# Performance work log

Measured on AMD Instinct MI355X. Metric: run time of the kernel, lower is better.

Reference implementation:

```python
import jax, jax.numpy as jnp
import numpy as np

WS = 8          # window size
DIM = 512       # midplanes
HEADS = 16      # 512 // 32
HD = DIM // HEADS
SCALE = HD ** -0.5
EPS = 1e-5      # BatchNorm eps


def _rel_index():
    # Swin-style relative position index, (WS*WS, WS*WS) int32, static.
    coords = np.stack(np.meshgrid(np.arange(WS), np.arange(WS), indexing='ij')).reshape(2, -1)
    rel = (coords[:, :, None] - coords[:, None, :]).transpose(1, 2, 0)
    rel[..., 0] += WS - 1
    rel[..., 1] += WS - 1
    rel[..., 0] *= 2 * WS - 1
    return jnp.asarray(rel.sum(-1), dtype=jnp.int32)

REL_IDX = _rel_index()


def _bn(x, gamma, beta, mean, var):
    # eval-mode BatchNorm2d on (B, C, H, W)
    inv = jax.lax.rsqrt(var + EPS)
    return (x - mean[None, :, None, None]) * (inv * gamma)[None, :, None, None] + beta[None, :, None, None]


def _forward(x, qkv_w, qkv_b, proj_w, proj_b, rel_bias_table,
             bn1_gamma, bn1_beta, bn1_mean, bn1_var,
             mlp_w1, mlp_b1, mlp_w2, mlp_b2,
             bn2_gamma, bn2_beta, bn2_mean, bn2_var):
    B, C, H, W = x.shape
    Hb, Wb = H // WS, W // WS
    shortcut = x

    xn = _bn(x, bn1_gamma, bn1_beta, bn1_mean, bn1_var)

    # window_partition (islocal=True): (B,C,H,W) -> (B*nW, WS*WS, C)
    xw = xn.reshape(B, C, Hb, WS, Wb, WS).transpose(0, 2, 4, 3, 5, 1).reshape(-1, WS * WS, C)

    # WindowAttention
    B_, N, _ = xw.shape
    qkv = xw @ qkv_w + qkv_b                       # (B_, N, 3*C)
    qkv = qkv.reshape(B_, N, 3, HEADS, HD).transpose(2, 0, 3, 1, 4)
    q, k, v = qkv[0], qkv[1], qkv[2]               # (B_, H, N, HD)
    attn = jnp.einsum('bhnd,bhmd->bhnm', q * SCALE, k)
    bias = rel_bias_table[REL_IDX]                 # (N, N, HEADS)
    attn = attn + bias.transpose(2, 0, 1)[None]
    attn = jax.nn.softmax(attn, axis=-1)
    out = jnp.einsum('bhnm,bhmd->bhnd', attn, v).transpose(0, 2, 1, 3).reshape(B_, N, C)
    out = out @ proj_w + proj_b                    # (B_, N, C)

    # window_reverse (islocal=True) — replicate torch's .view reinterpretation exactly
    aw = out.reshape(-1, WS, WS, DIM)              # (B*nW, WS, WS, C) contiguous
    xr = aw.reshape(B, DIM, Hb, Wb, WS, WS)        # row-major reinterpret (as in torch .view)
    xr = xr.transpose(0, 1, 2, 4, 3, 5).reshape(B, DIM, H, W)

    x1 = shortcut + xr                             # drop_path is identity at eval

    # MLP of 1x1 convs
    xn2 = _bn(x1, bn2_gamma, bn2_beta, bn2_mean, bn2_var)
    h = jnp.einsum('oc,bchw->bohw', mlp_w1, xn2) + mlp_b1[None, :, None, None]
    h = jax.nn.gelu(h, approximate=False)
    h = jnp.einsum('oc,bchw->bohw', mlp_w2, h) + mlp_b2[None, :, None, None]
    return x1 + h


def setup_inputs() -> dict:
    key = jax.random.key(0)
    ks = jax.random.split(key, 12)
    B, H, W = 8, 128, 128
    s = 0.02
    return {
        'x': jax.random.normal(ks[0], (B, DIM, H, W), dtype=jnp.float32),
        'qkv_w': jax.random.normal(ks[1], (DIM, 3 * DIM), dtype=jnp.float32) * s,
        'qkv_b': jnp.zeros((3 * DIM,), jnp.float32),
        'proj_w': jax.random.normal(ks[2], (DIM, DIM), dtype=jnp.float32) * s,
        'proj_b': jnp.zeros((DIM,), jnp.float32),
        'rel_bias_table': jax.random.normal(ks[3], ((2 * WS - 1) ** 2, HEADS), dtype=jnp.float32) * s,
        'bn1_gamma': jnp.ones((DIM,), jnp.float32),
        'bn1_beta': jnp.zeros((DIM,), jnp.float32),
        'bn1_mean': jax.random.normal(ks[4], (DIM,), dtype=jnp.float32) * 0.1,
        'bn1_var': jax.random.uniform(ks[5], (DIM,), jnp.float32, 0.5, 1.5),
        'mlp_w1': jax.random.normal(ks[6], (DIM, DIM), dtype=jnp.float32) * s,
        'mlp_b1': jnp.zeros((DIM,), jnp.float32),
        'mlp_w2': jax.random.normal(ks[7], (DIM, DIM), dtype=jnp.float32) * s,
        'mlp_b2': jnp.zeros((DIM,), jnp.float32),
        'bn2_gamma': jnp.ones((DIM,), jnp.float32),
        'bn2_beta': jnp.zeros((DIM,), jnp.float32),
        'bn2_mean': jax.random.normal(ks[8], (DIM,), dtype=jnp.float32) * 0.1,
        'bn2_var': jax.random.uniform(ks[9], (DIM,), jnp.float32, 0.5, 1.5),
    }


def reference(x, qkv_w, qkv_b, proj_w, proj_b, rel_bias_table,
              bn1_gamma, bn1_beta, bn1_mean, bn1_var,
              mlp_w1, mlp_b1, mlp_w2, mlp_b2,
              bn2_gamma, bn2_beta, bn2_mean, bn2_var):
    return _forward(x, qkv_w, qkv_b, proj_w, proj_b, rel_bias_table,
                    bn1_gamma, bn1_beta, bn1_mean, bn1_var,
                    mlp_w1, mlp_b1, mlp_w2, mlp_b2,
                    bn2_gamma, bn2_beta, bn2_mean, bn2_var)
```

## Files before the change

kernel.cpp:

```cpp
#include <hip/hip_runtime.h>
#include <cstddef>


typedef unsigned short ushort_t;
typedef __attribute__((ext_vector_type(8))) short short8;
typedef __attribute__((ext_vector_type(4))) float float4v;

__device__ __forceinline__ float bf2f(unsigned short h) {
  union { unsigned int u; float f; } c; c.u = ((unsigned int)h) << 16; return c.f;
}
__device__ __forceinline__ unsigned short f2bf(float f) {
  union { float f; unsigned int u; } c; c.f = f;
  unsigned int u = c.u;
  unsigned int r = u + 0x7fffu + ((u >> 16) & 1u);
  return (unsigned short)(r >> 16);
}
__device__ __forceinline__ void async16(const void* g, void* l) {
  __builtin_amdgcn_global_load_lds(
      (const __attribute__((address_space(1))) unsigned int*)g,
      (__attribute__((address_space(3))) unsigned int*)l, 16, 0, 0);
}

__global__ void transpose_cast(const float* __restrict__ W, ushort_t* __restrict__ Wt,
                               int K, int N) {
  int idx = blockIdx.x * 256 + threadIdx.x;
  if (idx >= K * N) return;
  int nn = idx / K, kk = idx - nn * K;
  Wt[idx] = f2bf(W[(size_t)kk * N + nn]);
}
__global__ void cast_bf(const float* __restrict__ W, ushort_t* __restrict__ Wt, int total) {
  int idx = blockIdx.x * 256 + threadIdx.x;
  if (idx < total) Wt[idx] = f2bf(W[idx]);
}

__global__ __launch_bounds__(256) void prep_qkv(
    const float* __restrict__ x, const float* __restrict__ gamma,
    const float* __restrict__ beta, const float* __restrict__ mean,
    const float* __restrict__ var, ushort_t* __restrict__ A0) {
  const int w = blockIdx.x;
  const int cc0 = blockIdx.y << 5;
  const int b = w >> 8, hb = (w >> 4) & 15, wb = w & 15;
  __shared__ __align__(16) ushort_t tile[64][32];
  const int tid = threadIdx.x;
  const int ci = tid >> 3, row = tid & 7;
  const int c = cc0 + ci;
  const float a = gamma[c] * rsqrtf(var[c] + 1e-5f);
  const float sh = beta[c] - mean[c] * a;
  const float* xp = x + (((size_t)b * 512 + c) * 128 + (hb << 3) + row) * 128 + (wb << 3);
#pragma unroll
  for (int j = 0; j < 8; ++j) tile[(row << 3) + j][ci] = f2bf(xp[j] * a + sh);
  __syncthreads();
  const int n = tid >> 2, d0 = (tid & 3) << 3;
  *(uint4*)(A0 + (size_t)((w << 6) + n) * 512 + cc0 + d0) = *(const uint4*)&tile[n][d0];
}

template <int EPI>
__global__ __launch_bounds__(256) void gemm_bt(
    const ushort_t* __restrict__ A, const ushort_t* __restrict__ Bt,
    const float* __restrict__ bias, ushort_t* __restrict__ C,
    int M, int N, int K) {
  __shared__ __align__(16) ushort_t lA[128 * 32];
  __shared__ __align__(16) ushort_t lB[128 * 32];
  const int tid = threadIdx.x;
  const int wave = tid >> 6, lane = tid & 63;
  const int m0 = blockIdx.y << 7, n0 = blockIdx.x << 7;
  const int wm = (wave & 1) << 6, wn = (wave >> 1) << 6;

  float4v acc[4][4];
#pragma unroll
  for (int i = 0; i < 4; ++i)
#pragma unroll
    for (int j = 0; j < 4; ++j)
#pragma unroll
      for (int r = 0; r < 4; ++r) acc[i][j][r] = 0.0f;

  const int srow = (wave << 5) + (lane >> 2);
  const int skb = (lane & 3) << 3;
  const ushort_t* Ag = A + (size_t)(m0 + srow) * K + skb;
  const ushort_t* Bg = Bt + (size_t)(n0 + srow) * K + skb;
  ushort_t* lA0 = &lA[(wave << 5) * 32];
  ushort_t* lA1 = &lA[((wave << 5) + 16) * 32];
  ushort_t* lB0 = &lB[(wave << 5) * 32];
  ushort_t* lB1 = &lB[((wave << 5) + 16) * 32];
  const int fr = lane & 15;
  const int fk = (lane >> 4) << 3;

  for (int kt = 0; kt < K; kt += 32) {
    async16(Ag + kt, lA0);
    async16(Ag + kt + (size_t)16 * K, lA1);
    async16(Bg + kt, lB0);
    async16(Bg + kt + (size_t)16 * K, lB1);
    __syncthreads();
    short8 af[4], bfr[4];
#pragma unroll
    for (int i = 0; i < 4; ++i) {
      af[i] = *(const short8*)&lA[(wm + (i << 4) + fr) * 32 + fk];
      bfr[i] = *(const short8*)&lB[(wn + (i << 4) + fr) * 32 + fk];
    }
#pragma unroll
    for (int i = 0; i < 4; ++i)
#pragma unroll
      for (int j = 0; j < 4; ++j)
        acc[i][j] = __builtin_amdgcn_mfma_f32_16x16x32_bf16(af[i], bfr[j], acc[i][j], 0, 0, 0);
    __syncthreads();
  }

  const int cr = (lane >> 4) << 2;
  const int cc = lane & 15;
#pragma unroll
  for (int j = 0; j < 4; ++j) {
    const int col = n0 + wn + (j << 4) + cc;
    const float bv = bias[col];
#pragma unroll
    for (int i = 0; i < 4; ++i) {
      size_t base = (size_t)(m0 + wm + (i << 4) + cr) * N + col;
#pragma unroll
      for (int r = 0; r < 4; ++r) {
        float v = acc[i][j][r] + bv;
        if (EPI == 1) v = 0.5f * v * (1.0f + erff(v * 0.70710678118654752f));
        C[base + (size_t)r * N] = f2bf(v);
      }
    }
  }
}

__global__ __launch_bounds__(256) void attn_kernel(
    const ushort_t* __restrict__ QKV, const float* __restrict__ table,
    ushort_t* __restrict__ OUT) {
  const int w = blockIdx.x;
  const int h = blockIdx.y;
  __shared__ __align__(16) ushort_t Vt[32][72];
  __shared__ __align__(16) ushort_t Pw[4][16][72];
  __shared__ float bias_s[225];
  const int tid = threadIdx.x;
  const int wave = tid >> 6, lane = tid & 63;
  const int g = lane >> 4, c = lane & 15;

  if (tid < 225) bias_s[tid] = table[tid * 16 + h];

  const ushort_t* base = QKV + (size_t)(w << 6) * 1536 + h * 32;

  {
    uint4 vv = *(const uint4*)(base + (size_t)lane * 1536 + 1024 + (wave << 3));
    const ushort_t* vp = (const ushort_t*)&vv;
#pragma unroll
    for (int e = 0; e < 8; ++e) Vt[(wave << 3) + e][lane] = vp[e];
  }

  short8 qf = *(const short8*)(base + (size_t)((wave << 4) + c) * 1536 + (g << 3));
  short8 kf[4];
#pragma unroll
  for (int j = 0; j < 4; ++j)
    kf[j] = *(const short8*)(base + (size_t)((j << 4) + c) * 1536 + 512 + (g << 3));

  float4v acc[4];
#pragma unroll
  for (int j = 0; j < 4; ++j) {
#pragma unroll
    for (int r = 0; r < 4; ++r) acc[j][r] = 0.0f;
    acc[j] = __builtin_amdgcn_mfma_f32_16x16x32_bf16(qf, kf[j], acc[j], 0, 0, 0);
  }

  __syncthreads();

  const int q0 = (wave << 4) + (g << 2);
#pragma unroll
  for (int j = 0; j < 4; ++j) {
    const int k = (j << 4) + c;
    const int r2 = k >> 3, c2 = k & 7;
#pragma unroll
    for (int r = 0; r < 4; ++r) {
      const int q = q0 + r;
      const int idx = ((q >> 3) - r2 + 7) * 15 + ((q & 7) - c2 + 7);
      acc[j][r] = acc[j][r] * 0.17677669529663689f + bias_s[idx];
    }
  }

#pragma unroll
  for (int r = 0; r < 4; ++r) {
    float m = fmaxf(fmaxf(acc[0][r], acc[1][r]), fmaxf(acc[2][r], acc[3][r]));
    m = fmaxf(m, __shfl_xor(m, 1));
    m = fmaxf(m, __shfl_xor(m, 2));
    m = fmaxf(m, __shfl_xor(m, 4));
    m = fmaxf(m, __shfl_xor(m, 8));
    float s = 0.0f;
#pragma unroll
    for (int j = 0; j < 4; ++j) { acc[j][r] = __expf(acc[j][r] - m); s += acc[j][r]; }
    s += __shfl_xor(s, 1);
    s += __shfl_xor(s, 2);
    s += __shfl_xor(s, 4);
    s += __shfl_xor(s, 8);
    const float inv = 1.0f / s;
#pragma unroll
    for (int j = 0; j < 4; ++j)
      Pw[wave][(g << 2) + r][(j << 4) + c] = f2bf(acc[j][r] * inv);
  }

  __syncthreads();

  float4v oacc[2];
#pragma unroll
  for (int j2 = 0; j2 < 2; ++j2)
#pragma unroll
    for (int r = 0; r < 4; ++r) oacc[j2][r] = 0.0f;
#pragma unroll
  for (int ks = 0; ks < 2; ++ks) {
    short8 pa = *(const short8*)&Pw[wave][c][(ks << 5) + (g << 3)];
#pragma unroll
    for (int j2 = 0; j2 < 2; ++j2) {
      short8 vb = *(const short8*)&Vt[(j2 << 4) + c][(ks << 5) + (g << 3)];
      oacc[j2] = __builtin_amdgcn_mfma_f32_16x16x32_bf16(pa, vb, oacc[j2], 0, 0, 0);
    }
  }

  ushort_t* op = OUT + (size_t)((w << 6) + (wave << 4)) * 512 + h * 32;
#pragma unroll
  for (int j2 = 0; j2 < 2; ++j2)
#pragma unroll
    for (int r = 0; r < 4; ++r)
      op[(size_t)((g << 2) + r) * 512 + (j2 << 4) + c] = f2bf(oacc[j2][r]);
}

__device__ __forceinline__ size_t scramble_idx(int b, int F) {
  const int hb0 = F >> 19, wb0 = (F >> 15) & 15;
  const int rr = (F >> 12) & 7, ccol = (F >> 9) & 7, ch = F & 511;
  return ((size_t)(b * 256 + hb0 * 16 + wb0) * 64 + rr * 8 + ccol) * 512 + ch;
}

__global__ __launch_bounds__(256) void prep_mlp(
    const float* __restrict__ x, const ushort_t* __restrict__ PROJ,
    const float* __restrict__ gamma, const float* __restrict__ beta,
    const float* __restrict__ mean, const float* __restrict__ var,
    ushort_t* __restrict__ XN2) {
  const int pc = blockIdx.x;
  const int cc0 = blockIdx.y << 5;
  const int p0 = pc << 6;
  const int b = p0 >> 14, hh = (p0 >> 7) & 127;
  __shared__ __align__(16) ushort_t tile[64][32];
  const int tid = threadIdx.x;
  const int ci = tid >> 3, wg = (tid & 7) << 3;
  const int c = cc0 + ci;
  const float a = gamma[c] * rsqrtf(var[c] + 1e-5f);
  const float sh = beta[c] - mean[c] * a;
  const int w0 = (p0 & 127) + wg;
  const float* xp = x + (((size_t)b * 512 + c) * 128 + hh) * 128 + w0;
  const int hb = hh >> 3, r2 = hh & 7;
#pragma unroll
  for (int j = 0; j < 8; ++j) {
    const int ww = w0 + j;
    const int F = (c << 14) + (hb << 10) + ((ww >> 3) << 6) + (r2 << 3) + (ww & 7);
    const float x1 = xp[j] + bf2f(PROJ[scramble_idx(b, F)]);
    tile[wg + j][ci] = f2bf(x1 * a + sh);
  }
  __syncthreads();
  const int i2 = tid >> 2, d0 = (tid & 3) << 3;
  *(uint4*)(XN2 + (size_t)(p0 + i2) * 512 + cc0 + d0) = *(const uint4*)&tile[i2][d0];
}

__global__ __launch_bounds__(256) void final_add(
    const float* __restrict__ x, const ushort_t* __restrict__ PROJ,
    const ushort_t* __restrict__ H2, float* __restrict__ out) {
  const int pc = blockIdx.x, cc0 = blockIdx.y << 5;
  const int p0 = pc << 6;
  const int b = p0 >> 14, hh = (p0 >> 7) & 127;
  __shared__ float tile[32][65];
  const int tid = threadIdx.x;
  {
    const int i2 = tid >> 2, d0 = (tid & 3) << 3;
    const ushort_t* hp = H2 + (size_t)(p0 + i2) * 512 + cc0 + d0;
#pragma unroll
    for (int j = 0; j < 8; ++j) tile[d0 + j][i2] = bf2f(hp[j]);
  }
  __syncthreads();
  const int ci = tid >> 3, wg = (tid & 7) << 3;
  const int c = cc0 + ci;
  const int w0 = (p0 & 127) + wg;
  const float* xp = x + (((size_t)b * 512 + c) * 128 + hh) * 128 + w0;
  float* op = out + (((size_t)b * 512 + c) * 128 + hh) * 128 + w0;
  const int hb = hh >> 3, r2 = hh & 7;
#pragma unroll
  for (int j = 0; j < 8; ++j) {
    const int ww = w0 + j;
    const int F = (c << 14) + (hb << 10) + ((ww >> 3) << 6) + (r2 << 3) + (ww & 7);
    op[j] = xp[j] + bf2f(PROJ[scramble_idx(b, F)]) + tile[ci][wg + j];
  }
}

extern "C" void kernel_launch(void* const* d_in, const int* in_sizes, int n_in,
                              void* d_out, int out_size, void* d_ws, size_t ws_size,
                              hipStream_t stream) {
  const float* x      = (const float*)d_in[0];
  const float* qkv_w  = (const float*)d_in[1];
  const float* qkv_b  = (const float*)d_in[2];
  const float* proj_w = (const float*)d_in[3];
  const float* proj_b = (const float*)d_in[4];
  const float* rel_t  = (const float*)d_in[5];
  const float* bn1g = (const float*)d_in[6];
  const float* bn1b = (const float*)d_in[7];
  const float* bn1m = (const float*)d_in[8];
  const float* bn1v = (const float*)d_in[9];
  const float* w1 = (const float*)d_in[10];
  const float* b1 = (const float*)d_in[11];
  const float* w2 = (const float*)d_in[12];
  const float* b2 = (const float*)d_in[13];
  const float* bn2g = (const float*)d_in[14];
  const float* bn2b = (const float*)d_in[15];
  const float* bn2m = (const float*)d_in[16];
  const float* bn2v = (const float*)d_in[17];
  float* out = (float*)d_out;

  char* ws = (char*)d_ws;
  const size_t SZ = (size_t)131072 * 512 * 2;
  ushort_t* WQKV  = (ushort_t*)(ws);
  ushort_t* WPROJ = (ushort_t*)(ws + 1572864);
  ushort_t* W1B   = (ushort_t*)(ws + 2097152);
  ushort_t* W2B   = (ushort_t*)(ws + 2621440);
  ushort_t* A0    = (ushort_t*)(ws + 3145728);
  ushort_t* QKV   = (ushort_t*)(ws + 3145728 + SZ);
  ushort_t* OUTB  = A0;
  ushort_t* PROJ  = QKV;
  ushort_t* XN2   = (ushort_t*)((char*)QKV + SZ);
  ushort_t* H1    = (ushort_t*)((char*)QKV + 2 * SZ);
  ushort_t* H2    = A0;

  transpose_cast<<<(512 * 1536 + 255) / 256, 256, 0, stream>>>(qkv_w, WQKV, 512, 1536);
  transpose_cast<<<(512 * 512 + 255) / 256, 256, 0, stream>>>(proj_w, WPROJ, 512, 512);
  cast_bf<<<(512 * 512 + 255) / 256, 256, 0, stream>>>(w1, W1B, 512 * 512);
  cast_bf<<<(512 * 512 + 255) / 256, 256, 0, stream>>>(w2, W2B, 512 * 512);

  prep_qkv<<<dim3(2048, 16), 256, 0, stream>>>(x, bn1g, bn1b, bn1m, bn1v, A0);
  gemm_bt<0><<<dim3(12, 1024), 256, 0, stream>>>(A0, WQKV, qkv_b, QKV, 131072, 1536, 512);
  attn_kernel<<<dim3(2048, 16), 256, 0, stream>>>(QKV, rel_t, OUTB);
  gemm_bt<0><<<dim3(4, 1024), 256, 0, stream>>>(OUTB, WPROJ, proj_b, PROJ, 131072, 512, 512);
  prep_mlp<<<dim3(2048, 16), 256, 0, stream>>>(x, PROJ, bn2g, bn2b, bn2m, bn2v, XN2);
  gemm_bt<1><<<dim3(4, 1024), 256, 0, stream>>>(XN2, W1B, b1, H1, 131072, 512, 512);
  gemm_bt<0><<<dim3(4, 1024), 256, 0, stream>>>(H1, W2B, b2, H2, 131072, 512, 512);
  final_add<<<dim3(2048, 16), 256, 0, stream>>>(x, PROJ, H2, out);
}
```

Baseline: 1.933 ms.

## Replace GEMM with 256x256 double-buffered 8-wave kernel with XCD swizzle

```diff
diff --git a/kernel.cpp b/kernel.cpp
--- a/kernel.cpp
+++ b/kernel.cpp
@@ -20,6 +20,10 @@
       (const __attribute__((address_space(1))) unsigned int*)g,
       (__attribute__((address_space(3))) unsigned int*)l, 16, 0, 0);
 }
+
+#define BAR() asm volatile("s_barrier" ::: "memory")
+#define WAITV6() asm volatile("s_waitcnt vmcnt(6)" ::: "memory")
+#define WAITV0() asm volatile("s_waitcnt vmcnt(0)" ::: "memory")
 
 __global__ void transpose_cast(const float* __restrict__ W, ushort_t* __restrict__ Wt,
                                int K, int N) {
@@ -54,71 +58,169 @@
   *(uint4*)(A0 + (size_t)((w << 6) + n) * 512 + cc0 + d0) = *(const uint4*)&tile[n][d0];
 }
 
+#define QUAD(BB, MH, NH)                                                        \
+  __builtin_amdgcn_s_setprio(1);                                                \
+  _Pragma("unroll")                                                             \
+  for (int mi = 0; mi < 4; ++mi) {                                              \
+    _Pragma("unroll")                                                           \
+    for (int nj = 0; nj < 2; ++nj) {                                            \
+      _Pragma("unroll")                                                         \
+      for (int kk = 0; kk < 2; ++kk)                                            \
+        acc[(MH * 4) + mi][(NH * 2) + nj] =                                     \
+            __builtin_amdgcn_mfma_f32_16x16x32_bf16(                            \
+                a[mi][kk], BB[nj][kk], acc[(MH * 4) + mi][(NH * 2) + nj], 0, 0, 0); \
+    }                                                                           \
+  }                                                                             \
+  __builtin_amdgcn_s_setprio(0);
+
 template <int EPI>
-__global__ __launch_bounds__(256) void gemm_bt(
+__global__ __launch_bounds__(512, 2) void gemm256(
     const ushort_t* __restrict__ A, const ushort_t* __restrict__ Bt,
     const float* __restrict__ bias, ushort_t* __restrict__ C,
     int M, int N, int K) {
-  __shared__ __align__(16) ushort_t lA[128 * 32];
-  __shared__ __align__(16) ushort_t lB[128 * 32];
+  __shared__ __align__(16) ushort_t smem[65536];
+  ushort_t* A0L = smem;
+  ushort_t* B0L = smem + 16384;
+  ushort_t* A1L = smem + 32768;
+  ushort_t* B1L = smem + 49152;
+
   const int tid = threadIdx.x;
-  const int wave = tid >> 6, lane = tid & 63;
-  const int m0 = blockIdx.y << 7, n0 = blockIdx.x << 7;
-  const int wm = (wave & 1) << 6, wn = (wave >> 1) << 6;
-
-  float4v acc[4][4];
-#pragma unroll
-  for (int i = 0; i < 4; ++i)
+  const int wid = tid >> 6, lane = tid & 63;
+
+  const int gx = gridDim.x;
+  const int nwg = gx * gridDim.y;
+  const int orig = blockIdx.y * gx + blockIdx.x;
+  const int q = nwg >> 3, r = nwg & 7;
+  const int xcd = orig & 7, lid = orig >> 3;
+  const int swz = (xcd < r ? xcd * (q + 1) : r * (q + 1) + (xcd - r) * q) + lid;
+  const int by = swz / gx, bx = swz - by * gx;
+  const int m0 = by << 8, n0 = bx << 8;
+
+  const int NT = K >> 6;
+  const int NI = NT >> 1;
+
+  const int sseg = (lane & 7) ^ (lane >> 3);
+  auto stA = [&](ushort_t* dst, int stripe, int kt) {
+#pragma unroll
+    for (int j = 0; j < 2; ++j) {
+      const int pr = (j << 7) + (stripe << 6) + (wid << 3);
+      async16(A + (size_t)(m0 + pr + (lane >> 3)) * K + (kt << 6) + (sseg << 3),
+              dst + ((size_t)pr << 6));
+    }
+  };
+  auto stB = [&](ushort_t* dst, int stripe, int kt) {
+#pragma unroll
+    for (int j = 0; j < 2; ++j) {
+      const int pr = (j << 7) + ((wid >> 2) << 6) + (stripe << 5) + ((wid & 3) << 3);
+      async16(Bt + (size_t)(n0 + pr + (lane >> 3)) * K + (kt << 6) + (sseg << 3),
+              dst + ((size_t)pr << 6));
+    }
+  };
+
+  const int fr = lane & 15, kg = lane >> 4;
+  const int wr = wid >> 2, wc = wid & 3;
+  const int ar0 = (wr << 7) + fr;
+  const int br0 = (wc << 6) + fr;
+  const int sx = fr & 7;
+  auto ldA = [&](const ushort_t* buf, int mi_abs, int kk) -> short8 {
+    const int row = ar0 + (mi_abs << 4);
+    const int seg = ((kk << 2) + kg) ^ sx;
+    return *(const short8*)(buf + (row << 6) + (seg << 3));
+  };
+  auto ldB = [&](const ushort_t* buf, int ni_abs, int kk) -> short8 {
+    const int row = br0 + (ni_abs << 4);
+    const int seg = ((kk << 2) + kg) ^ sx;
+    return *(const short8*)(buf + (row << 6) + (seg << 3));
+  };
+
+  short8 a[4][2], b0[2][2], b1[2][2];
+  float4v acc[8][4];
+#pragma unroll
+  for (int i = 0; i < 8; ++i)
 #pragma unroll
     for (int j = 0; j < 4; ++j)
 #pragma unroll
-      for (int r = 0; r < 4; ++r) acc[i][j][r] = 0.0f;
-
-  const int srow = (wave << 5) + (lane >> 2);
-  const int skb = (lane & 3) << 3;
-  const ushort_t* Ag = A + (size_t)(m0 + srow) * K + skb;
-  const ushort_t* Bg = Bt + (size_t)(n0 + srow) * K + skb;
-  ushort_t* lA0 = &lA[(wave << 5) * 32];
-  ushort_t* lA1 = &lA[((wave << 5) + 16) * 32];
-  ushort_t* lB0 = &lB[(wave << 5) * 32];
-  ushort_t* lB1 = &lB[((wave << 5) + 16) * 32];
-  const int fr = lane & 15;
-  const int fk = (lane >> 4) << 3;
-
-  for (int kt = 0; kt < K; kt += 32) {
-    async16(Ag + kt, lA0);
-    async16(Ag + kt + (size_t)16 * K, lA1);
-    async16(Bg + kt, lB0);
-    async16(Bg + kt + (size_t)16 * K, lB1);
-    __syncthreads();
-    short8 af[4], bfr[4];
-#pragma unroll
-    for (int i = 0; i < 4; ++i) {
-      af[i] = *(const short8*)&lA[(wm + (i << 4) + fr) * 32 + fk];
-      bfr[i] = *(const short8*)&lB[(wn + (i << 4) + fr) * 32 + fk];
-    }
-#pragma unroll
-    for (int i = 0; i < 4; ++i)
-#pragma unroll
-      for (int j = 0; j < 4; ++j)
-        acc[i][j] = __builtin_amdgcn_mfma_f32_16x16x32_bf16(af[i], bfr[j], acc[i][j], 0, 0, 0);
-    __syncthreads();
-  }
-
-  const int cr = (lane >> 4) << 2;
-  const int cc = lane & 15;
-#pragma unroll
-  for (int j = 0; j < 4; ++j) {
-    const int col = n0 + wn + (j << 4) + cc;
+      for (int rr = 0; rr < 4; ++rr) acc[i][j][rr] = 0.0f;
+
+  stA(A0L, 0, 0);
+  stB(B0L, 0, 0);
+  stB(B0L, 1, 0);
+  stA(A0L, 1, 0);
+  stA(A1L, 0, 1);
+  stB(B1L, 1, 1);
+  stA(A1L, 1, 1);
+  WAITV6();
+  BAR();
+
+  for (int i = 0; i < NI; ++i) {
+    const int ktB = 2 * i + 1;
+    const int kt2 = 2 * i + 2, kt3 = 2 * i + 3;
+    const bool st = (kt2 < NT);
+#pragma unroll
+    for (int mi = 0; mi < 4; ++mi) { a[mi][0] = ldA(A0L, mi, 0); a[mi][1] = ldA(A0L, mi, 1); }
+#pragma unroll
+    for (int nj = 0; nj < 2; ++nj) { b0[nj][0] = ldB(B0L, nj, 0); b0[nj][1] = ldB(B0L, nj, 1); }
+    stB(B1L, 0, ktB);
+    BAR();
+    QUAD(b0, 0, 0);
+    BAR();
+#pragma unroll
+    for (int nj = 0; nj < 2; ++nj) { b1[nj][0] = ldB(B0L, 2 + nj, 0); b1[nj][1] = ldB(B0L, 2 + nj, 1); }
+    if (st) stA(A0L, 0, kt2);
+    BAR();
+    QUAD(b1, 0, 1);
+    BAR();
+#pragma unroll
+    for (int mi = 0; mi < 4; ++mi) { a[mi][0] = ldA(A0L, 4 + mi, 0); a[mi][1] = ldA(A0L, 4 + mi, 1); }
+    if (st) stB(B0L, 1, kt2);
+    BAR();
+    QUAD(b1, 1, 1);
+    BAR();
+    if (st) stA(A0L, 1, kt2);
+    BAR();
+    QUAD(b0, 1, 0);
+    if (st) { WAITV6(); } else { WAITV0(); }
+    BAR();
+#pragma unroll
+    for (int mi = 0; mi < 4; ++mi) { a[mi][0] = ldA(A1L, mi, 0); a[mi][1] = ldA(A1L, mi, 1); }
+#pragma unroll
+    for (int nj = 0; nj < 2; ++nj) { b0[nj][0] = ldB(B1L, nj, 0); b0[nj][1] = ldB(B1L, nj, 1); }
+    if (st) stB(B0L, 0, kt2);
+    BAR();
+    QUAD(b0, 0, 0);
+    BAR();
+#pragma unroll
+    for (int nj = 0; nj < 2; ++nj) { b1[nj][0] = ldB(B1L, 2 + nj, 0); b1[nj][1] = ldB(B1L, 2 + nj, 1); }
+    if (st) stA(A1L, 0, kt3);
+    BAR();
+    QUAD(b1, 0, 1);
+    BAR();
+#pragma unroll
+    for (int mi = 0; mi < 4; ++mi) { a[mi][0] = ldA(A1L, 4 + mi, 0); a[mi][1] = ldA(A1L, 4 + mi, 1); }
+    if (st) stB(B1L, 1, kt3);
+    BAR();
+    QUAD(b1, 1, 1);
+    BAR();
+    if (st) stA(A1L, 1, kt3);
+    BAR();
+    QUAD(b0, 1, 0);
+    if (st) { WAITV6(); }
+    BAR();
+  }
+
+  const int cr = kg << 2;
+#pragma unroll
+  for (int ni = 0; ni < 4; ++ni) {
+    const int col = n0 + (wc << 6) + (ni << 4) + fr;
     const float bv = bias[col];
 #pragma unroll
-    for (int i = 0; i < 4; ++i) {
-      size_t base = (size_t)(m0 + wm + (i << 4) + cr) * N + col;
-#pragma unroll
-      for (int r = 0; r < 4; ++r) {
-        float v = acc[i][j][r] + bv;
+    for (int mi = 0; mi < 8; ++mi) {
+      const size_t base = (size_t)(m0 + (wr << 7) + (mi << 4) + cr) * N + col;
+#pragma unroll
+      for (int rr = 0; rr < 4; ++rr) {
+        float v = acc[mi][ni][rr] + bv;
         if (EPI == 1) v = 0.5f * v * (1.0f + erff(v * 0.70710678118654752f));
-        C[base + (size_t)r * N] = f2bf(v);
+        C[base + (size_t)rr * N] = f2bf(v);
       }
     }
   }
@@ -170,8 +272,8 @@
     const int r2 = k >> 3, c2 = k & 7;
 #pragma unroll
     for (int r = 0; r < 4; ++r) {
-      const int q = q0 + r;
-      const int idx = ((q >> 3) - r2 + 7) * 15 + ((q & 7) - c2 + 7);
+      const int qq = q0 + r;
+      const int idx = ((qq >> 3) - r2 + 7) * 15 + ((qq & 7) - c2 + 7);
       acc[j][r] = acc[j][r] * 0.17677669529663689f + bias_s[idx];
     }
   }
@@ -329,11 +431,11 @@
   cast_bf<<<(512 * 512 + 255) / 256, 256, 0, stream>>>(w2, W2B, 512 * 512);
 
   prep_qkv<<<dim3(2048, 16), 256, 0, stream>>>(x, bn1g, bn1b, bn1m, bn1v, A0);
-  gemm_bt<0><<<dim3(12, 1024), 256, 0, stream>>>(A0, WQKV, qkv_b, QKV, 131072, 1536, 512);
+  gemm256<0><<<dim3(6, 512), 512, 0, stream>>>(A0, WQKV, qkv_b, QKV, 131072, 1536, 512);
   attn_kernel<<<dim3(2048, 16), 256, 0, stream>>>(QKV, rel_t, OUTB);
-  gemm_bt<0><<<dim3(4, 1024), 256, 0, stream>>>(OUTB, WPROJ, proj_b, PROJ, 131072, 512, 512);
+  gemm256<0><<<dim3(2, 512), 512, 0, stream>>>(OUTB, WPROJ, proj_b, PROJ, 131072, 512, 512);
   prep_mlp<<<dim3(2048, 16), 256, 0, stream>>>(x, PROJ, bn2g, bn2b, bn2m, bn2v, XN2);
-  gemm_bt<1><<<dim3(4, 1024), 256, 0, stream>>>(XN2, W1B, b1, H1, 131072, 512, 512);
-  gemm_bt<0><<<dim3(4, 1024), 256, 0, stream>>>(H1, W2B, b2, H2, 131072, 512, 512);
+  gemm256<1><<<dim3(2, 512), 512, 0, stream>>>(XN2, W1B, b1, H1, 131072, 512, 512);
+  gemm256<0><<<dim3(2, 512), 512, 0, stream>>>(H1, W2B, b2, H2, 131072, 512, 512);
   final_add<<<dim3(2048, 16), 256, 0, stream>>>(x, PROJ, H2, out);
 }
```

New measurement: 1.750 ms. 9.5% less time.
